# Optimization experiments

Measured on AMD Instinct MI355X. Metric: run time of the kernel, lower is better.

Reference implementation:

```python
import jax, jax.numpy as jnp
import numpy as np

B, T, H, E, D, K = 4, 4096, 2048, 8, 1024, 2

def setup_inputs() -> dict:
    key = jax.random.key(0)
    ks = jax.random.split(key, 7)
    x  = jax.random.normal(ks[0], (B, T, H), dtype=jnp.float32)
    Wr = jax.random.normal(ks[1], (H, E), dtype=jnp.float32) * (1.0 / np.sqrt(H))
    br = jnp.zeros((E,), dtype=jnp.float32)
    We = jax.random.normal(ks[2], (E, H, D), dtype=jnp.float32) * (1.0 / np.sqrt(H))
    be = jnp.zeros((E, D), dtype=jnp.float32)
    Wc = jax.random.normal(ks[3], (D, H), dtype=jnp.float32) * (1.0 / np.sqrt(D))
    bc = jnp.zeros((H,), dtype=jnp.float32)
    return {"x": x, "Wr": Wr, "br": br, "We": We, "be": be, "Wc": Wc, "bc": bc}

def reference(x, Wr, br, We, be, Wc, bc):
    # Router: [B,T,H] @ [H,E] -> [B,T,E]
    router_logits = jnp.einsum('bth,he->bte', x, Wr) + br
    scores = jax.nn.softmax(router_logits, axis=-1)
    # top-k over experts (sorted descending, like torch.topk)
    topk_scores, topk_idx = jax.lax.top_k(scores, K)  # [B,T,K]
    # Dense all-expert linear: [B,T,E,D]
    expert_outs = jnp.einsum('bth,ehd->bted', x, We) + be
    # Gather the chosen experts per token: [B,T,K,D]
    gather_idx = jnp.broadcast_to(topk_idx[..., None], (B, T, K, D))
    chosen = jnp.take_along_axis(expert_outs, gather_idx, axis=2)
    # Weighted sum over top-k: [B,T,D]
    weighted = jnp.sum(chosen * topk_scores[..., None], axis=2)
    # Combine: [B,T,D] @ [D,H] -> [B,T,H]
    return jnp.einsum('btd,dh->bth', weighted, Wc) + bc
```

## Files before the change

kernel.cpp:

```cpp
#include <hip/hip_runtime.h>
#include <hip/hip_bf16.h>

typedef float f32x4 __attribute__((ext_vector_type(4)));
typedef short bf16x8 __attribute__((ext_vector_type(8)));

#define M_NT 16
#define M_OFF 17
#define M_TBL 32
#define MAX_TILES 136
#define NCHUNK 1024

__device__ __forceinline__ void gload16(const void* g, void* l) {
  __builtin_amdgcn_global_load_lds(
      (const __attribute__((address_space(1))) void*)g,
      (__attribute__((address_space(3))) void*)l, 16, 0, 0);
}

__device__ __forceinline__ float bf2f(unsigned short u) {
  union { unsigned int i; float f; } v; v.i = ((unsigned int)u) << 16; return v.f;
}
__device__ __forceinline__ unsigned short f2bf(float f) {
  __hip_bfloat16 h = __float2bfloat16(f);
  return __builtin_bit_cast(unsigned short, h);
}

#define CBAR() do { asm volatile("" ::: "memory"); __builtin_amdgcn_s_barrier(); asm volatile("" ::: "memory"); } while (0)
#define VMC3() asm volatile("s_waitcnt vmcnt(3)" ::: "memory")
#define VMC0() asm volatile("s_waitcnt vmcnt(0)" ::: "memory")

__global__ void transpose_cvt(const float* __restrict__ src,
                              unsigned short* __restrict__ dst, int R, int C) {
  __shared__ float tile[32][33];
  int b = blockIdx.z;
  int c0 = blockIdx.x * 32, r0 = blockIdx.y * 32;
  src += (size_t)b * R * C;
  dst += (size_t)b * R * C;
  int tx = threadIdx.x, ty = threadIdx.y;
#pragma unroll
  for (int i = 0; i < 32; i += 8)
    tile[ty + i][tx] = src[(size_t)(r0 + ty + i) * C + c0 + tx];
  __syncthreads();
#pragma unroll
  for (int i = 0; i < 32; i += 8)
    dst[(size_t)(c0 + ty + i) * R + r0 + tx] = f2bf(tile[tx][ty + i]);
}

__global__ __launch_bounds__(256) void router_kernel(
    const float* __restrict__ x, const float* __restrict__ Wr,
    const float* __restrict__ br, unsigned short* __restrict__ xbf,
    float* __restrict__ scores, int* __restrict__ idx,
    int* __restrict__ blk_hist) {
  __shared__ int cnt[8];
  int tid = threadIdx.x, lane = tid & 63, w = tid >> 6;
  if (tid < 8) cnt[tid] = 0;
  __syncthreads();
  int t0 = blockIdx.x * 16 + w * 4;
  const float* xr = x + (size_t)t0 * 2048;
  unsigned short* xo = xbf + (size_t)t0 * 2048;
  float acc[4][8] = {};
#pragma unroll
  for (int j = 0; j < 8; ++j) {
    int h0 = j * 256 + lane * 4;
    float4 xv[4];
#pragma unroll
    for (int t = 0; t < 4; ++t) xv[t] = *(const float4*)(xr + (size_t)t * 2048 + h0);
#pragma unroll
    for (int t = 0; t < 4; ++t) {
      ushort4 p;
      p.x = f2bf(xv[t].x); p.y = f2bf(xv[t].y);
      p.z = f2bf(xv[t].z); p.w = f2bf(xv[t].w);
      *(ushort4*)(xo + (size_t)t * 2048 + h0) = p;
    }
    const float4* wp = (const float4*)(Wr + (size_t)h0 * 8);
#pragma unroll
    for (int c = 0; c < 4; ++c) {
      float4 w0 = wp[2 * c], w1 = wp[2 * c + 1];
      float xc0 = (c == 0) ? xv[0].x : (c == 1) ? xv[0].y : (c == 2) ? xv[0].z : xv[0].w;
      float xc1 = (c == 0) ? xv[1].x : (c == 1) ? xv[1].y : (c == 2) ? xv[1].z : xv[1].w;
      float xc2 = (c == 0) ? xv[2].x : (c == 1) ? xv[2].y : (c == 2) ? xv[2].z : xv[2].w;
      float xc3 = (c == 0) ? xv[3].x : (c == 1) ? xv[3].y : (c == 2) ? xv[3].z : xv[3].w;
      acc[0][0] += xc0 * w0.x; acc[0][1] += xc0 * w0.y; acc[0][2] += xc0 * w0.z; acc[0][3] += xc0 * w0.w;
      acc[0][4] += xc0 * w1.x; acc[0][5] += xc0 * w1.y; acc[0][6] += xc0 * w1.z; acc[0][7] += xc0 * w1.w;
      acc[1][0] += xc1 * w0.x; acc[1][1] += xc1 * w0.y; acc[1][2] += xc1 * w0.z; acc[1][3] += xc1 * w0.w;
      acc[1][4] += xc1 * w1.x; acc[1][5] += xc1 * w1.y; acc[1][6] += xc1 * w1.z; acc[1][7] += xc1 * w1.w;
      acc[2][0] += xc2 * w0.x; acc[2][1] += xc2 * w0.y; acc[2][2] += xc2 * w0.z; acc[2][3] += xc2 * w0.w;
      acc[2][4] += xc2 * w1.x; acc[2][5] += xc2 * w1.y; acc[2][6] += xc2 * w1.z; acc[2][7] += xc2 * w1.w;
      acc[3][0] += xc3 * w0.x; acc[3][1] += xc3 * w0.y; acc[3][2] += xc3 * w0.z; acc[3][3] += xc3 * w0.w;
      acc[3][4] += xc3 * w1.x; acc[3][5] += xc3 * w1.y; acc[3][6] += xc3 * w1.z; acc[3][7] += xc3 * w1.w;
    }
  }
#pragma unroll
  for (int t = 0; t < 4; ++t)
#pragma unroll
    for (int e = 0; e < 8; ++e)
#pragma unroll
      for (int off = 32; off > 0; off >>= 1)
        acc[t][e] += __shfl_xor(acc[t][e], off);
  if (lane < 4) {
    int t = t0 + lane;
    float l[8];
#pragma unroll
    for (int e = 0; e < 8; ++e) {
      float v = (lane == 0) ? acc[0][e] : (lane == 1) ? acc[1][e]
              : (lane == 2) ? acc[2][e] : acc[3][e];
      l[e] = v + br[e];
    }
    float mx = l[0];
#pragma unroll
    for (int e = 1; e < 8; ++e) mx = fmaxf(mx, l[e]);
    float se = 0.f;
#pragma unroll
    for (int e = 0; e < 8; ++e) se += __expf(l[e] - mx);
    float inv = 1.f / se;
    int e1 = 0; float b1 = l[0];
#pragma unroll
    for (int e = 1; e < 8; ++e) if (l[e] > b1) { b1 = l[e]; e1 = e; }
    int e2 = -1; float b2 = -1e30f;
#pragma unroll
    for (int e = 0; e < 8; ++e) if (e != e1 && l[e] > b2) { b2 = l[e]; e2 = e; }
    idx[2 * t] = e1; idx[2 * t + 1] = e2;
    scores[2 * t] = __expf(b1 - mx) * inv;
    scores[2 * t + 1] = __expf(b2 - mx) * inv;
    atomicAdd(&cnt[e1], 1);
    atomicAdd(&cnt[e2], 1);
  }
  __syncthreads();
  if (tid < 8) blk_hist[blockIdx.x * 8 + tid] = cnt[tid];
}

__global__ __launch_bounds__(512) void scan_kernel(
    const int* __restrict__ blk_hist, int* __restrict__ chunk_base,
    int* __restrict__ meta, int* __restrict__ rowlist) {
  __shared__ int stot[8], soff[8];
  int tid = threadIdx.x, lane = tid & 63, e = tid >> 6;
  int running = 0;
  for (int g = 0; g < NCHUNK / 64; ++g) {
    int c = g * 64 + lane;
    int v = blk_hist[c * 8 + e];
    int orig = v;
#pragma unroll
    for (int off = 1; off < 64; off <<= 1) {
      int n = __shfl_up(v, off);
      if (lane >= off) v += n;
    }
    chunk_base[c * 8 + e] = running + v - orig;
    running += __shfl(v, 63);
  }
  if (lane == 0) stot[e] = running;
  __syncthreads();
  if (tid == 0) {
    int off = 0, nt = 0;
    int4* tbl = (int4*)(meta + M_TBL);
    for (int ee = 0; ee < 8; ++ee) {
      int c = stot[ee];
      meta[M_OFF + ee] = off; soff[ee] = off;
      int tiles = (c + 255) >> 8;
      for (int t = 0; t < tiles; ++t)
        tbl[nt++] = make_int4(ee, off + t * 256, min(256, c - t * 256), 0);
      off += tiles << 8;
    }
    meta[M_NT] = nt;
  }
  __syncthreads();
  for (int ee = 0; ee < 8; ++ee) {
    int c = stot[ee], end = ((c + 255) >> 8) << 8;
    for (int i = c + tid; i < end; i += 512) rowlist[soff[ee] + i] = 0;
  }
}

__global__ void scatter_kernel(const int* __restrict__ idx,
                               const int* __restrict__ chunk_base,
                               const int* __restrict__ meta,
                               int* __restrict__ rowlist) {
  int c = blockIdx.x, lane = threadIdx.x;
  int entry = c * 32 + lane;
  int e = (lane < 32) ? idx[entry] : -1;
#pragma unroll
  for (int ee = 0; ee < 8; ++ee) {
    unsigned long long m = __ballot(e == ee);
    if (e == ee) {
      int rank = __popcll(m & ((1ull << lane) - 1));
      rowlist[meta[M_OFF + ee] + chunk_base[c * 8 + ee] + rank] = entry;
    }
  }
}


#define RD_FRAGS(AB, BB) do { \
  _Pragma("unroll") for (int m_ = 0; m_ < 4; ++m_) \
    av[m_] = *(const bf16x8*)(aP + (AB) + m_ * 1024); \
  _Pragma("unroll") for (int n_ = 0; n_ < 4; ++n_) \
    bv[n_] = *(const bf16x8*)(bP + (BB) + n_ * 1024); \
} while (0)

#define MFMA16() do { \
  __builtin_amdgcn_s_setprio(1); \
  _Pragma("unroll") for (int m_ = 0; m_ < 4; ++m_) \
  _Pragma("unroll") for (int n_ = 0; n_ < 4; ++n_) \
    acc[m_][n_] = __builtin_amdgcn_mfma_f32_16x16x32_bf16(av[m_], bv[n_], acc[m_][n_], 0, 0, 0); \
  __builtin_amdgcn_s_setprio(0); \
} while (0)

#define STAGE(BUFB, KOFF) do { \
  gload16(pA0 + (KOFF), dA + (BUFB)); \
  gload16(pA1 + (KOFF), dA + (BUFB) + 8192); \
  gload16(pB0 + (KOFF), dBs + (BUFB)); \
} while (0)

__global__ __launch_bounds__(512, 4) void expert_gemm(
    const unsigned short* __restrict__ xbf,
    const unsigned short* __restrict__ WeT,
    const float* __restrict__ be,
    const float* __restrict__ scores,
    const int* __restrict__ rowlist,
    const int* __restrict__ meta,
    unsigned short* __restrict__ z) {
  __shared__ char smem[49152];
  __shared__ int lrows[256];
  int nt = meta[M_NT];
  int flat = blockIdx.y * 8 + blockIdx.x;
  int work = (flat & 7) * 136 + (flat >> 3);
  int tileid = work >> 3, nb = work & 7;
  if (tileid >= nt) return;
  int4 tt = ((const int4*)(meta + M_TBL))[tileid];
  int e = tt.x, base = tt.y, valid = tt.z;
  int n0 = nb * 128;
  int tid = threadIdx.x, lane = tid & 63, w = tid >> 6;
  if (tid < 256) lrows[tid] = rowlist[base + tid];
  __syncthreads();
  int wm = w >> 1, wn = w & 1;
  int fl = lane & 15, q = lane >> 4;
  int rA = tid >> 2;
  int sl = ((tid & 3) ^ ((rA >> 1) & 3)) * 16;
  const char* pA0 = (const char*)xbf + (size_t)(lrows[rA] >> 1) * 4096 + sl;
  const char* pA1 = (const char*)xbf + (size_t)(lrows[rA + 128] >> 1) * 4096 + sl;
  const char* pB0 = (const char*)WeT + ((size_t)e * 1024 + n0 + rA) * 4096 + sl;
  char* dA  = smem + tid * 16;
  char* dBs = smem + 16384 + tid * 16;
  int swz = ((fl >> 1) & 3) << 4;
  const char* aP = smem + (wm * 64 + fl) * 64 + ((q * 16) ^ swz);
  const char* bP = smem + 16384 + (wn * 64 + fl) * 64 + ((q * 16) ^ swz);
  STAGE(0, 0); STAGE(24576, 64);
  VMC3(); CBAR();
  f32x4 acc[4][4] = {};
  bf16x8 av[4], bv[4];
  const int NT = 64;
  for (int t2 = 0; t2 < NT; t2 += 2) {
    int koff = t2 * 64;
    RD_FRAGS(0, 0);
    MFMA16();
    CBAR();
    if (t2 + 2 < NT) { STAGE(0, koff + 128); VMC3(); } else { VMC0(); }
    CBAR();
    RD_FRAGS(24576, 24576);
    MFMA16();
    CBAR();
    if (t2 + 3 < NT) { STAGE(24576, koff + 192); VMC3(); } else { VMC0(); }
    CBAR();
  }
  float bev[4];
#pragma unroll
  for (int nc = 0; nc < 4; ++nc)
    bev[nc] = be[e * 1024 + n0 + wn * 64 + nc * 16 + fl];
#pragma unroll
  for (int mi = 0; mi < 4; ++mi) {
    int rowbase = wm * 64 + mi * 16 + q * 4;
#pragma unroll
    for (int r = 0; r < 4; ++r) {
      int row = rowbase + r;
      if (row < valid) {
        int entry = lrows[row];
        float s = scores[entry];
        unsigned short* zr = z + (size_t)entry * 1024 + n0 + wn * 64 + fl;
#pragma unroll
        for (int nc = 0; nc < 4; ++nc)
          zr[nc * 16] = f2bf((acc[mi][nc][r] + bev[nc]) * s);
      }
    }
  }
}

__global__ __launch_bounds__(512, 4) void combine_gemm(
    const unsigned short* __restrict__ y,
    const unsigned short* __restrict__ WcT,
    const float* __restrict__ bc,
    float* __restrict__ out) {
  __shared__ char smem[49152];
  int flat = blockIdx.y * 8 + blockIdx.x;
  int work = (flat & 7) * 128 + (flat >> 3);
  int mtile = work >> 4, nb = work & 15;
  int m0 = mtile * 256, n0 = nb * 128;
  int tid = threadIdx.x, lane = tid & 63, w = tid >> 6;
  int wm = w >> 1, wn = w & 1;
  int fl = lane & 15, q = lane >> 4;
  int rA = tid >> 2;
  int sl = ((tid & 3) ^ ((rA >> 1) & 3)) * 16;
  const char* pA0 = (const char*)y + (size_t)(m0 + rA) * 2048 + sl;
  const char* pA1 = (const char*)y + (size_t)(m0 + rA + 128) * 2048 + sl;
  const char* pB0 = (const char*)WcT + (size_t)(n0 + rA) * 2048 + sl;
  char* dA  = smem + tid * 16;
  char* dBs = smem + 16384 + tid * 16;
  int swz = ((fl >> 1) & 3) << 4;
  const char* aP = smem + (wm * 64 + fl) * 64 + ((q * 16) ^ swz);
  const char* bP = smem + 16384 + (wn * 64 + fl) * 64 + ((q * 16) ^ swz);
  STAGE(0, 0); STAGE(24576, 64);
  VMC3(); CBAR();
  f32x4 acc[4][4] = {};
  bf16x8 av[4], bv[4];
  const int NT = 32;
  for (int t2 = 0; t2 < NT; t2 += 2) {
    int koff = t2 * 64;
    RD_FRAGS(0, 0);
    MFMA16();
    CBAR();
    if (t2 + 2 < NT) { STAGE(0, koff + 128); VMC3(); } else { VMC0(); }
    CBAR();
    RD_FRAGS(24576, 24576);
    MFMA16();
    CBAR();
    if (t2 + 3 < NT) { STAGE(24576, koff + 192); VMC3(); } else { VMC0(); }
    CBAR();
  }
  float bcv[4];
#pragma unroll
  for (int nc = 0; nc < 4; ++nc)
    bcv[nc] = bc[n0 + wn * 64 + nc * 16 + fl];
#pragma unroll
  for (int mi = 0; mi < 4; ++mi) {
    int rowbase = m0 + wm * 64 + mi * 16 + q * 4;
#pragma unroll
    for (int r = 0; r < 4; ++r) {
      float* orow = out + (size_t)(rowbase + r) * 2048 + n0 + wn * 64 + fl;
#pragma unroll
      for (int nc = 0; nc < 4; ++nc)
        orow[nc * 16] = acc[mi][nc][r] + bcv[nc];
    }
  }
}

__global__ void wsum_kernel(const unsigned short* __restrict__ z,
                            unsigned short* __restrict__ y) {
  size_t i = ((size_t)blockIdx.x * 256 + threadIdx.x) * 8;
  size_t t = i >> 10, d = i & 1023;
  int4 za = *(const int4*)(z + (t * 2) * 1024 + d);
  int4 zb = *(const int4*)(z + (t * 2 + 1) * 1024 + d);
  int4 r;
  const unsigned short* pa = (const unsigned short*)&za;
  const unsigned short* pb = (const unsigned short*)&zb;
  unsigned short* pr = (unsigned short*)&r;
#pragma unroll
  for (int j = 0; j < 8; ++j) pr[j] = f2bf(bf2f(pa[j]) + bf2f(pb[j]));
  *(int4*)(y + i) = r;
}

extern "C" void kernel_launch(void* const* d_in, const int* in_sizes, int n_in,
                              void* d_out, int out_size, void* d_ws, size_t ws_size,
                              hipStream_t stream) {
  const float* x  = (const float*)d_in[0];
  const float* Wr = (const float*)d_in[1];
  const float* br = (const float*)d_in[2];
  const float* We = (const float*)d_in[3];
  const float* be = (const float*)d_in[4];
  const float* Wc = (const float*)d_in[5];
  const float* bc = (const float*)d_in[6];
  float* out = (float*)d_out;

  char* ws = (char*)d_ws;
  size_t o = 0;
  auto alloc = [&](size_t b) {
    char* p = ws + o;
    o = (o + b + 255) & ~(size_t)255;
    return p;
  };
  unsigned short* xbf = (unsigned short*)alloc(16384UL * 2048 * 2);
  unsigned short* WeT = (unsigned short*)alloc(8UL * 1024 * 2048 * 2);
  unsigned short* WcT = (unsigned short*)alloc(2048UL * 1024 * 2);
  unsigned short* z   = (unsigned short*)alloc(32768UL * 1024 * 2);
  unsigned short* yw  = (unsigned short*)alloc(16384UL * 1024 * 2);
  float* scores = (float*)alloc(32768UL * 4);
  int* idx      = (int*)alloc(32768UL * 4);
  int* rowlist  = (int*)alloc(36864UL * 4);
  int* meta     = (int*)alloc(8192);
  int* blk_hist = (int*)alloc(NCHUNK * 8 * 4);
  int* chunk_base = (int*)alloc(NCHUNK * 8 * 4);
  (void)ws_size; (void)in_sizes; (void)n_in; (void)out_size;

  hipLaunchKernelGGL(transpose_cvt, dim3(32, 64, 8), dim3(32, 8), 0, stream, We, WeT, 2048, 1024);
  hipLaunchKernelGGL(transpose_cvt, dim3(64, 32, 1), dim3(32, 8), 0, stream, Wc, WcT, 1024, 2048);
  hipLaunchKernelGGL(router_kernel, dim3(NCHUNK), dim3(256), 0, stream, x, Wr, br, xbf, scores, idx, blk_hist);
  hipLaunchKernelGGL(scan_kernel, dim3(1), dim3(512), 0, stream, blk_hist, chunk_base, meta, rowlist);
  hipLaunchKernelGGL(scatter_kernel, dim3(NCHUNK), dim3(64), 0, stream, idx, chunk_base, meta, rowlist);
  hipLaunchKernelGGL(expert_gemm, dim3(8, MAX_TILES), dim3(512), 0, stream,
                     xbf, WeT, be, scores, rowlist, meta, z);
  hipLaunchKernelGGL(wsum_kernel, dim3(8192), dim3(256), 0, stream, z, yw);
  hipLaunchKernelGGL(combine_gemm, dim3(8, 128), dim3(512), 0, stream, yw, WcT, bc, out);
}
```

Before: 384.3 us.

## Shrink expert and combine GEMM tiles from 256x128 to 128x128 with 256 threads

Both the expert GEMM and the combine GEMM move from 256x128 output tiles on 512-thread blocks to 128x128 tiles on 256-thread blocks. Shared memory per block drops from 48KB to 32KB, and each thread now issues four loads per stage instead of three, so the wait count changes to match. The scan builds 128-row tiles per expert, MAX_TILES is raised, and the grids double. The aim is less padding waste on partial expert tiles, more resident blocks per CU and better load balance, at the cost of lower per-block data reuse and more global traffic for B.

```diff
diff --git a/kernel.cpp b/kernel.cpp
--- a/kernel.cpp
+++ b/kernel.cpp
@@ -7,7 +7,7 @@
 #define M_NT 16
 #define M_OFF 17
 #define M_TBL 32
-#define MAX_TILES 136
+#define MAX_TILES 264
 #define NCHUNK 1024
 
 __device__ __forceinline__ void gload16(const void* g, void* l) {
@@ -25,7 +25,7 @@
 }
 
 #define CBAR() do { asm volatile("" ::: "memory"); __builtin_amdgcn_s_barrier(); asm volatile("" ::: "memory"); } while (0)
-#define VMC3() asm volatile("s_waitcnt vmcnt(3)" ::: "memory")
+#define VMC4() asm volatile("s_waitcnt vmcnt(4)" ::: "memory")
 #define VMC0() asm volatile("s_waitcnt vmcnt(0)" ::: "memory")
 
 __global__ void transpose_cvt(const float* __restrict__ src,
@@ -154,16 +154,16 @@
     for (int ee = 0; ee < 8; ++ee) {
       int c = stot[ee];
       meta[M_OFF + ee] = off; soff[ee] = off;
-      int tiles = (c + 255) >> 8;
+      int tiles = (c + 127) >> 7;
       for (int t = 0; t < tiles; ++t)
-        tbl[nt++] = make_int4(ee, off + t * 256, min(256, c - t * 256), 0);
-      off += tiles << 8;
+        tbl[nt++] = make_int4(ee, off + t * 128, min(128, c - t * 128), 0);
+      off += tiles << 7;
     }
     meta[M_NT] = nt;
   }
   __syncthreads();
   for (int ee = 0; ee < 8; ++ee) {
-    int c = stot[ee], end = ((c + 255) >> 8) << 8;
+    int c = stot[ee], end = ((c + 127) >> 7) << 7;
     for (int i = c + tid; i < end; i += 512) rowlist[soff[ee] + i] = 0;
   }
 }
@@ -186,11 +186,11 @@
 }
 
 
-#define RD_FRAGS(AB, BB) do { \
+#define RD_FRAGS(BUFB) do { \
   _Pragma("unroll") for (int m_ = 0; m_ < 4; ++m_) \
-    av[m_] = *(const bf16x8*)(aP + (AB) + m_ * 1024); \
+    av[m_] = *(const bf16x8*)(aP + (BUFB) + m_ * 1024); \
   _Pragma("unroll") for (int n_ = 0; n_ < 4; ++n_) \
-    bv[n_] = *(const bf16x8*)(bP + (BB) + n_ * 1024); \
+    bv[n_] = *(const bf16x8*)(bP + (BUFB) + n_ * 1024); \
 } while (0)
 
 #define MFMA16() do { \
@@ -203,11 +203,12 @@
 
 #define STAGE(BUFB, KOFF) do { \
   gload16(pA0 + (KOFF), dA + (BUFB)); \
-  gload16(pA1 + (KOFF), dA + (BUFB) + 8192); \
-  gload16(pB0 + (KOFF), dBs + (BUFB)); \
+  gload16(pA1 + (KOFF), dA + (BUFB) + 4096); \
+  gload16(pB0 + (KOFF), dB + (BUFB)); \
+  gload16(pB1 + (KOFF), dB + (BUFB) + 4096); \
 } while (0)
 
-__global__ __launch_bounds__(512, 4) void expert_gemm(
+__global__ __launch_bounds__(256, 4) void expert_gemm(
     const unsigned short* __restrict__ xbf,
     const unsigned short* __restrict__ WeT,
     const float* __restrict__ be,
@@ -215,47 +216,48 @@
     const int* __restrict__ rowlist,
     const int* __restrict__ meta,
     unsigned short* __restrict__ z) {
-  __shared__ char smem[49152];
-  __shared__ int lrows[256];
+  __shared__ char smem[32768];
+  __shared__ int lrows[128];
   int nt = meta[M_NT];
   int flat = blockIdx.y * 8 + blockIdx.x;
-  int work = (flat & 7) * 136 + (flat >> 3);
+  int work = (flat & 7) * MAX_TILES + (flat >> 3);
   int tileid = work >> 3, nb = work & 7;
   if (tileid >= nt) return;
   int4 tt = ((const int4*)(meta + M_TBL))[tileid];
   int e = tt.x, base = tt.y, valid = tt.z;
   int n0 = nb * 128;
   int tid = threadIdx.x, lane = tid & 63, w = tid >> 6;
-  if (tid < 256) lrows[tid] = rowlist[base + tid];
+  if (tid < 128) lrows[tid] = rowlist[base + tid];
   __syncthreads();
   int wm = w >> 1, wn = w & 1;
   int fl = lane & 15, q = lane >> 4;
   int rA = tid >> 2;
   int sl = ((tid & 3) ^ ((rA >> 1) & 3)) * 16;
   const char* pA0 = (const char*)xbf + (size_t)(lrows[rA] >> 1) * 4096 + sl;
-  const char* pA1 = (const char*)xbf + (size_t)(lrows[rA + 128] >> 1) * 4096 + sl;
+  const char* pA1 = (const char*)xbf + (size_t)(lrows[rA + 64] >> 1) * 4096 + sl;
   const char* pB0 = (const char*)WeT + ((size_t)e * 1024 + n0 + rA) * 4096 + sl;
-  char* dA  = smem + tid * 16;
-  char* dBs = smem + 16384 + tid * 16;
+  const char* pB1 = (const char*)WeT + ((size_t)e * 1024 + n0 + rA + 64) * 4096 + sl;
+  char* dA = smem + tid * 16;
+  char* dB = smem + 8192 + tid * 16;
   int swz = ((fl >> 1) & 3) << 4;
   const char* aP = smem + (wm * 64 + fl) * 64 + ((q * 16) ^ swz);
-  const char* bP = smem + 16384 + (wn * 64 + fl) * 64 + ((q * 16) ^ swz);
-  STAGE(0, 0); STAGE(24576, 64);
-  VMC3(); CBAR();
+  const char* bP = smem + 8192 + (wn * 64 + fl) * 64 + ((q * 16) ^ swz);
+  STAGE(0, 0); STAGE(16384, 64);
+  VMC4(); CBAR();
   f32x4 acc[4][4] = {};
   bf16x8 av[4], bv[4];
   const int NT = 64;
   for (int t2 = 0; t2 < NT; t2 += 2) {
     int koff = t2 * 64;
-    RD_FRAGS(0, 0);
+    RD_FRAGS(0);
     MFMA16();
     CBAR();
-    if (t2 + 2 < NT) { STAGE(0, koff + 128); VMC3(); } else { VMC0(); }
-    CBAR();
-    RD_FRAGS(24576, 24576);
+    if (t2 + 2 < NT) { STAGE(0, koff + 128); VMC4(); } else { VMC0(); }
+    CBAR();
+    RD_FRAGS(16384);
     MFMA16();
     CBAR();
-    if (t2 + 3 < NT) { STAGE(24576, koff + 192); VMC3(); } else { VMC0(); }
+    if (t2 + 3 < NT) { STAGE(16384, koff + 192); VMC4(); } else { VMC0(); }
     CBAR();
   }
   float bev[4];
@@ -280,45 +282,46 @@
   }
 }
 
-__global__ __launch_bounds__(512, 4) void combine_gemm(
+__global__ __launch_bounds__(256, 4) void combine_gemm(
     const unsigned short* __restrict__ y,
     const unsigned short* __restrict__ WcT,
     const float* __restrict__ bc,
     float* __restrict__ out) {
-  __shared__ char smem[49152];
+  __shared__ char smem[32768];
   int flat = blockIdx.y * 8 + blockIdx.x;
-  int work = (flat & 7) * 128 + (flat >> 3);
-  int mtile = work >> 4, nb = work & 15;
-  int m0 = mtile * 256, n0 = nb * 128;
+  int work = (flat & 7) * 256 + (flat >> 3);
+  int mt = work >> 4, nb = work & 15;
+  int m0 = mt * 128, n0 = nb * 128;
   int tid = threadIdx.x, lane = tid & 63, w = tid >> 6;
   int wm = w >> 1, wn = w & 1;
   int fl = lane & 15, q = lane >> 4;
   int rA = tid >> 2;
   int sl = ((tid & 3) ^ ((rA >> 1) & 3)) * 16;
   const char* pA0 = (const char*)y + (size_t)(m0 + rA) * 2048 + sl;
-  const char* pA1 = (const char*)y + (size_t)(m0 + rA + 128) * 2048 + sl;
+  const char* pA1 = (const char*)y + (size_t)(m0 + rA + 64) * 2048 + sl;
   const char* pB0 = (const char*)WcT + (size_t)(n0 + rA) * 2048 + sl;
-  char* dA  = smem + tid * 16;
-  char* dBs = smem + 16384 + tid * 16;
+  const char* pB1 = (const char*)WcT + (size_t)(n0 + rA + 64) * 2048 + sl;
+  char* dA = smem + tid * 16;
+  char* dB = smem + 8192 + tid * 16;
   int swz = ((fl >> 1) & 3) << 4;
   const char* aP = smem + (wm * 64 + fl) * 64 + ((q * 16) ^ swz);
-  const char* bP = smem + 16384 + (wn * 64 + fl) * 64 + ((q * 16) ^ swz);
-  STAGE(0, 0); STAGE(24576, 64);
-  VMC3(); CBAR();
+  const char* bP = smem + 8192 + (wn * 64 + fl) * 64 + ((q * 16) ^ swz);
+  STAGE(0, 0); STAGE(16384, 64);
+  VMC4(); CBAR();
   f32x4 acc[4][4] = {};
   bf16x8 av[4], bv[4];
   const int NT = 32;
   for (int t2 = 0; t2 < NT; t2 += 2) {
     int koff = t2 * 64;
-    RD_FRAGS(0, 0);
+    RD_FRAGS(0);
     MFMA16();
     CBAR();
-    if (t2 + 2 < NT) { STAGE(0, koff + 128); VMC3(); } else { VMC0(); }
-    CBAR();
-    RD_FRAGS(24576, 24576);
+    if (t2 + 2 < NT) { STAGE(0, koff + 128); VMC4(); } else { VMC0(); }
+    CBAR();
+    RD_FRAGS(16384);
     MFMA16();
     CBAR();
-    if (t2 + 3 < NT) { STAGE(24576, koff + 192); VMC3(); } else { VMC0(); }
+    if (t2 + 3 < NT) { STAGE(16384, koff + 192); VMC4(); } else { VMC0(); }
     CBAR();
   }
   float bcv[4];
@@ -390,8 +393,8 @@
   hipLaunchKernelGGL(router_kernel, dim3(NCHUNK), dim3(256), 0, stream, x, Wr, br, xbf, scores, idx, blk_hist);
   hipLaunchKernelGGL(scan_kernel, dim3(1), dim3(512), 0, stream, blk_hist, chunk_base, meta, rowlist);
   hipLaunchKernelGGL(scatter_kernel, dim3(NCHUNK), dim3(64), 0, stream, idx, chunk_base, meta, rowlist);
-  hipLaunchKernelGGL(expert_gemm, dim3(8, MAX_TILES), dim3(512), 0, stream,
+  hipLaunchKernelGGL(expert_gemm, dim3(8, MAX_TILES), dim3(256), 0, stream,
                      xbf, WeT, be, scores, rowlist, meta, z);
   hipLaunchKernelGGL(wsum_kernel, dim3(8192), dim3(256), 0, stream, z, yw);
-  hipLaunchKernelGGL(combine_gemm, dim3(8, 128), dim3(512), 0, stream, yw, WcT, bc, out);
-}
+  hipLaunchKernelGGL(combine_gemm, dim3(8, 256), dim3(256), 0, stream, yw, WcT, bc, out);
+}
```

New measurement: 389.0 us. No clear change (+1.2%).
